# Kernel optimization log

Hardware: AMD Instinct MI355X
Metric: run time of the kernel (lower is better)

Reference implementation:

```python
import jax, jax.numpy as jnp
import numpy as np

N_ATOMS = 393216   # 4096 molecules * ~96 atoms
N_FEAT = 128
NB_FILTER = 128
NB_AFFINE = 11     # max_deg(10) + 1 - min_deg(0)
BATCH = 4096


def setup_inputs() -> dict:
    key = jax.random.key(0)
    k1, k2, k3, k4 = jax.random.split(key, 4)
    atoms = jax.random.normal(k1, (N_ATOMS, N_FEAT), jnp.float32)
    # stacked per-degree affine weights (glorot-ish scale)
    W = jax.random.normal(k2, (NB_AFFINE, N_FEAT, NB_FILTER), jnp.float32) / jnp.sqrt(jnp.float32(N_FEAT))
    b = jax.random.normal(k3, (NB_AFFINE, NB_FILTER), jnp.float32) * 0.01
    # contiguous degree layout: deg_slice[k] = (start, count), atoms sorted by degree
    counts = np.full(NB_AFFINE, N_ATOMS // NB_AFFINE, dtype=np.int32)
    counts[-1] += N_ATOMS - counts.sum()
    starts = np.concatenate([[0], np.cumsum(counts)[:-1]]).astype(np.int32)
    deg_slice = jnp.asarray(np.stack([starts, counts], axis=1))  # (11, 2) int32
    membership = jax.random.randint(k4, (N_ATOMS,), 0, BATCH, dtype=jnp.int32)
    return {"atoms": atoms, "W": W, "b": b, "deg_slice": deg_slice,
            "membership": membership, "batch_size": BATCH}


def reference(atoms, W, b, deg_slice, membership, batch_size):
    # atoms: (N, F); W: (K, F, O); b: (K, O); deg_slice: (K, 2)
    n = atoms.shape[0]
    nb_affine = W.shape[0]
    # Per-atom degree index from contiguous deg_slice layout:
    # deg_idx[i] = number of degree blocks that end at or before atom i.
    ends = jnp.cumsum(deg_slice[:, 1])                     # (K,)
    idx = jnp.arange(n, dtype=ends.dtype)
    deg_idx = jnp.sum(idx[:, None] >= ends[None, :], axis=1)  # (N,)
    # Per-degree affine: each atom uses the (W, b) of its degree block.
    out = jnp.zeros((n, W.shape[2]), dtype=atoms.dtype)
    for k in range(nb_affine):  # fixed small structural loop (11 distinct weight sets)
        yk = atoms @ W[k] + b[k]
        out = out + jnp.where((deg_idx == k)[:, None], yk, jnp.zeros((), atoms.dtype))
    # graph_gather: dynamic_partition + per-partition reduce_sum + concat == segment_sum
    pooled = jax.ops.segment_sum(out, membership, num_segments=batch_size)  # (B, O)
    # activation is 'linear' (identity); dropout is None
    return pooled
```

## Files before the change

### kernel.cpp

```cpp
#include <hip/hip_runtime.h>
#include <hip/hip_bf16.h>


#define CAP 64

typedef short bf16x8 __attribute__((ext_vector_type(8)));
typedef float f32x4  __attribute__((ext_vector_type(4)));

__device__ __forceinline__ unsigned short f2bf(float f) {
    unsigned int u = __builtin_bit_cast(unsigned int, f);
    u += 0x7fffu + ((u >> 16) & 1u);
    return (unsigned short)(u >> 16);
}

__device__ __forceinline__ int deg_of(int i, const int* __restrict__ ds, int K) {
    int k = 0, end = 0;
    for (int kk = 0; kk < K; ++kk) { end += ds[2 * kk + 1]; k += (i >= end) ? 1 : 0; }
    return k;
}

__global__ __launch_bounds__(256) void k_fill_wconv(
    const int* __restrict__ mem, const int* __restrict__ ds,
    const float* __restrict__ W,
    unsigned* __restrict__ cnt, unsigned* __restrict__ slots,
    unsigned short* __restrict__ Wb, int N, int K, int nb)
{
    int bx = blockIdx.x;
    if (bx >= nb) {
        __shared__ unsigned short t[128 * 130];
        int k = bx - nb;
        const float* Wk = W + (size_t)k * 16384;
        unsigned short* Wbk = Wb + (size_t)k * 16384;
        for (int e = threadIdx.x; e < 16384; e += 256) {
            int f = e >> 7, c = e & 127;
            t[f * 130 + c] = f2bf(Wk[e]);
        }
        __syncthreads();
        for (int e = threadIdx.x; e < 16384; e += 256) {
            int c = e >> 7, f = e & 127;
            Wbk[e] = t[f * 130 + c];
        }
        return;
    }
    int i = bx * 256 + threadIdx.x;
    if (i >= N) return;
    int key = mem[i] * K + deg_of(i, ds, K);
    unsigned p = atomicAdd(&cnt[key], 1u);
    if (p < CAP) slots[(size_t)key * CAP + p] = (unsigned)i;
}

__device__ __forceinline__ float4 f4add(float4 a, float4 b) {
    return make_float4(a.x + b.x, a.y + b.y, a.z + b.z, a.w + b.w);
}

__global__ __launch_bounds__(256) void k_phaseA(
    const float* __restrict__ atoms,
    const unsigned* __restrict__ cnt,
    const unsigned* __restrict__ slots,
    unsigned short* __restrict__ S, int KB)
{
    int bin = blockIdx.x * 4 + (threadIdx.x >> 6);
    if (bin >= KB) return;
    int lane = threadIdx.x & 63;
    int rpar = lane >> 5;
    int f4   = lane & 31;
    int n = (int)cnt[bin];
    if (n > CAP) n = CAP;
    const unsigned* sl = slots + (size_t)bin * CAP;

    float4 A0 = make_float4(0.f, 0.f, 0.f, 0.f);
    float4 A1 = A0, A2 = A0, A3 = A0;
    int j = rpar;
    for (; j + 6 < n; j += 8) {
        unsigned r0 = sl[j], r1 = sl[j + 2], r2 = sl[j + 4], r3 = sl[j + 6];
        float4 v0 = *reinterpret_cast<const float4*>(atoms + (size_t)r0 * 128 + f4 * 4);
        float4 v1 = *reinterpret_cast<const float4*>(atoms + (size_t)r1 * 128 + f4 * 4);
        float4 v2 = *reinterpret_cast<const float4*>(atoms + (size_t)r2 * 128 + f4 * 4);
        float4 v3 = *reinterpret_cast<const float4*>(atoms + (size_t)r3 * 128 + f4 * 4);
        A0 = f4add(A0, v0); A1 = f4add(A1, v1);
        A2 = f4add(A2, v2); A3 = f4add(A3, v3);
    }
    for (; j < n; j += 2) {
        float4 v = *reinterpret_cast<const float4*>(atoms + (size_t)sl[j] * 128 + f4 * 4);
        A0 = f4add(A0, v);
    }
    float4 Sm = f4add(f4add(A0, A1), f4add(A2, A3));
    Sm.x += __shfl_xor(Sm.x, 32, 64);
    Sm.y += __shfl_xor(Sm.y, 32, 64);
    Sm.z += __shfl_xor(Sm.z, 32, 64);
    Sm.w += __shfl_xor(Sm.w, 32, 64);
    if (rpar == 0) {
        unsigned lo = (unsigned)f2bf(Sm.x) | ((unsigned)f2bf(Sm.y) << 16);
        unsigned hi = (unsigned)f2bf(Sm.z) | ((unsigned)f2bf(Sm.w) << 16);
        *reinterpret_cast<uint2*>(S + (size_t)bin * 128 + f4 * 4) = make_uint2(lo, hi);
    }
}

__global__ __launch_bounds__(64) void k_phaseB(
    const unsigned short* __restrict__ S,
    const unsigned short* __restrict__ Wb,
    const unsigned* __restrict__ cnt,
    const float* __restrict__ bias,
    float* __restrict__ out,
    int K)
{
    int bx   = blockIdx.x;
    int s0   = (bx >> 2) * 16;
    int c0   = (bx & 3) * 32;
    int lane = threadIdx.x;
    int quad = lane >> 4, cb = lane & 15;

    const int KD = K * 128;
    f32x4 acc0 = (f32x4){0.f, 0.f, 0.f, 0.f};
    f32x4 acc1 = (f32x4){0.f, 0.f, 0.f, 0.f};

    const unsigned short* Arow = S  + (size_t)(s0 + cb) * KD + quad * 8;
    const unsigned short* B0   = Wb + (size_t)(c0 + cb)      * 128 + quad * 8;
    const unsigned short* B1   = Wb + (size_t)(c0 + 16 + cb) * 128 + quad * 8;

    #pragma unroll 1
    for (int kk = 0; kk < K; ++kk) {
        #pragma unroll
        for (int k0 = 0; k0 < 128; k0 += 32) {
            bf16x8 a  = *reinterpret_cast<const bf16x8*>(Arow + kk * 128 + k0);
            bf16x8 b0 = *reinterpret_cast<const bf16x8*>(B0 + (size_t)kk * 16384 + k0);
            bf16x8 b1 = *reinterpret_cast<const bf16x8*>(B1 + (size_t)kk * 16384 + k0);
            acc0 = __builtin_amdgcn_mfma_f32_16x16x32_bf16(a, b0, acc0, 0, 0, 0);
            acc1 = __builtin_amdgcn_mfma_f32_16x16x32_bf16(a, b1, acc1, 0, 0, 0);
        }
    }
    #pragma unroll
    for (int reg = 0; reg < 4; ++reg) {
        int s = s0 + quad * 4 + reg;
        float b0s = 0.f, b1s = 0.f;
        for (int k = 0; k < K; ++k) {
            float c = (float)cnt[(size_t)s * K + k];
            b0s += c * bias[k * 128 + c0 + cb];
            b1s += c * bias[k * 128 + c0 + 16 + cb];
        }
        out[(size_t)s * 128 + c0 + cb]      = acc0[reg] + b0s;
        out[(size_t)s * 128 + c0 + 16 + cb] = acc1[reg] + b1s;
    }
}

#define TM 64
#define LDA 136
#define LDW 136
__global__ __launch_bounds__(256, 2) void degree_affine_pool(
    const float* __restrict__ atoms, const float* __restrict__ W,
    const float* __restrict__ bias, const int* __restrict__ deg_slice,
    const int* __restrict__ membership, float* __restrict__ out, int K)
{
    __shared__ unsigned short Alds[TM * LDA];
    __shared__ unsigned short Wlds[128 * LDW];
    const int bid = blockIdx.x, tid = threadIdx.x;
    int k = -1, tile = 0, acc_t = 0;
    for (int kk = 0; kk < K; ++kk) {
        int c = deg_slice[2 * kk + 1];
        int nt = (c + TM - 1) >> 6;
        if (k < 0 && bid < acc_t + nt) { k = kk; tile = bid - acc_t; }
        acc_t += nt;
    }
    if (k < 0) return;
    const int start = deg_slice[2 * k], cnt = deg_slice[2 * k + 1];
    const int row0 = start + tile * TM;
    const int rows_valid = min(TM, cnt - tile * TM);
    for (int e = tid; e < TM * 32; e += 256) {
        int r = e >> 5, f4 = e & 31;
        float4 v = make_float4(0.f, 0.f, 0.f, 0.f);
        if (r < rows_valid)
            v = *reinterpret_cast<const float4*>(atoms + (size_t)(row0 + r) * 128 + f4 * 4);
        unsigned lo = (unsigned)f2bf(v.x) | ((unsigned)f2bf(v.y) << 16);
        unsigned hi = (unsigned)f2bf(v.z) | ((unsigned)f2bf(v.w) << 16);
        *reinterpret_cast<uint2*>(&Alds[r * LDA + f4 * 4]) = make_uint2(lo, hi);
    }
    const float* Wk = W + (size_t)k * 16384;
    for (int e = tid; e < 8192; e += 256) {
        int c = e & 127, f2 = e >> 7;
        unsigned p = (unsigned)f2bf(Wk[(2 * f2) * 128 + c]) |
                     ((unsigned)f2bf(Wk[(2 * f2 + 1) * 128 + c]) << 16);
        *reinterpret_cast<unsigned*>(&Wlds[c * LDW + 2 * f2]) = p;
    }
    __syncthreads();
    const int wave = tid >> 6, lane = tid & 63, quad = lane >> 4, cb = lane & 15;
    f32x4 acc[8];
    #pragma unroll
    for (int ct = 0; ct < 8; ++ct) acc[ct] = (f32x4){0.f, 0.f, 0.f, 0.f};
    #pragma unroll
    for (int k0 = 0; k0 < 128; k0 += 32) {
        bf16x8 af = *reinterpret_cast<const bf16x8*>(&Alds[(wave * 16 + cb) * LDA + k0 + quad * 8]);
        #pragma unroll
        for (int ct = 0; ct < 8; ++ct) {
            bf16x8 bf = *reinterpret_cast<const bf16x8*>(&Wlds[(ct * 16 + cb) * LDW + k0 + quad * 8]);
            acc[ct] = __builtin_amdgcn_mfma_f32_16x16x32_bf16(af, bf, acc[ct], 0, 0, 0);
        }
    }
    int segs[4]; bool valid[4];
    #pragma unroll
    for (int reg = 0; reg < 4; ++reg) {
        int rl = wave * 16 + quad * 4 + reg;
        valid[reg] = (rl < rows_valid);
        segs[reg] = valid[reg] ? membership[row0 + rl] : 0;
    }
    const float* bk = bias + k * 128;
    #pragma unroll
    for (int ct = 0; ct < 8; ++ct) {
        int col = ct * 16 + cb;
        float bv = bk[col];
        #pragma unroll
        for (int reg = 0; reg < 4; ++reg)
            if (valid[reg])
                __hip_atomic_fetch_add(out + (size_t)segs[reg] * 128 + col,
                                       acc[ct][reg] + bv, __ATOMIC_RELAXED,
                                       __HIP_MEMORY_SCOPE_AGENT);
    }
}

static inline size_t aln(size_t x) { return (x + 255) & ~(size_t)255; }

extern "C" void kernel_launch(void* const* d_in, const int* in_sizes, int n_in,
                              void* d_out, int out_size, void* d_ws, size_t ws_size,
                              hipStream_t stream) {
    const float* atoms = (const float*)d_in[0];
    const float* W     = (const float*)d_in[1];
    const float* bias  = (const float*)d_in[2];
    const int*   deg   = (const int*)d_in[3];
    const int*   mem   = (const int*)d_in[4];
    float*       out   = (float*)d_out;

    const int K  = in_sizes[3] / 2;
    const int N  = in_sizes[0] / 128;
    const int B  = out_size / 128;
    const int KB = B * K;

    size_t oWb   = 0;                       size_t sWb   = (size_t)K * 16384 * 2;
    size_t oCnt  = aln(oWb + sWb);          size_t sCnt  = (size_t)KB * 4;
    size_t oSlot = aln(oCnt + sCnt);        size_t sSlot = (size_t)KB * CAP * 4;
    size_t oS    = aln(oSlot + sSlot);      size_t sS    = (size_t)KB * 128 * 2;
    size_t total = oS + sS;

    if (ws_size < total || (B & 15) != 0) {
        (void)hipMemsetAsync(d_out, 0, (size_t)out_size * sizeof(float), stream);
        const int blocks = (N + TM - 1) / TM + K;
        degree_affine_pool<<<blocks, 256, 0, stream>>>(atoms, W, bias, deg, mem, out, K);
        return;
    }

    char* ws = (char*)d_ws;
    unsigned short* Wb    = (unsigned short*)(ws + oWb);
    unsigned*       cnt   = (unsigned*)(ws + oCnt);
    unsigned*       slots = (unsigned*)(ws + oSlot);
    unsigned short* S     = (unsigned short*)(ws + oS);

    (void)hipMemsetAsync(cnt, 0, sCnt, stream);

    const int nb = (N + 255) / 256;
    k_fill_wconv<<<nb + K, 256, 0, stream>>>(mem, deg, W, cnt, slots, Wb, N, K, nb);
    k_phaseA    <<<(KB + 3) / 4, 256, 0, stream>>>(atoms, cnt, slots, S, KB);
    k_phaseB    <<<(B / 16) * 4, 64, 0, stream>>>(S, Wb, cnt, bias, out, K);
}
```

Baseline: 347.7 us.

## Fuse bin-fill, gather-sum and MFMA phases into one persistent kernel with grid barriers

Replaces three launches (fill/weight-convert, per-bin gather sum, MFMA GEMM) with one persistent 512-block kernel that separates the phases with atomic global barriers. The barrier counter is zeroed by the same memset as the counts. Slot indices for each bin are staged in LDS before the gather loop. The aim is to remove launch gaps and tail effects between kernels. The cost is fewer waves per phase, barrier spin overhead, and reliance on all 512 blocks being co-resident, which could deadlock if they are not.

Result: slower. 654.1 us (+88.1%).

```diff
diff --git a/kernel.cpp b/kernel.cpp
--- a/kernel.cpp
+++ b/kernel.cpp
@@ -2,7 +2,9 @@
 #include <hip/hip_bf16.h>
 
 
-#define CAP 64
+#define CAP  64
+#define GRID 512
+#define TPB  256
 
 typedef short bf16x8 __attribute__((ext_vector_type(8)));
 typedef float f32x4  __attribute__((ext_vector_type(4)));
@@ -19,127 +21,138 @@
     return k;
 }
 
-__global__ __launch_bounds__(256) void k_fill_wconv(
-    const int* __restrict__ mem, const int* __restrict__ ds,
-    const float* __restrict__ W,
-    unsigned* __restrict__ cnt, unsigned* __restrict__ slots,
-    unsigned short* __restrict__ Wb, int N, int K, int nb)
-{
-    int bx = blockIdx.x;
-    if (bx >= nb) {
-        __shared__ unsigned short t[128 * 130];
-        int k = bx - nb;
-        const float* Wk = W + (size_t)k * 16384;
-        unsigned short* Wbk = Wb + (size_t)k * 16384;
-        for (int e = threadIdx.x; e < 16384; e += 256) {
-            int f = e >> 7, c = e & 127;
-            t[f * 130 + c] = f2bf(Wk[e]);
-        }
-        __syncthreads();
-        for (int e = threadIdx.x; e < 16384; e += 256) {
-            int c = e >> 7, f = e & 127;
-            Wbk[e] = t[f * 130 + c];
-        }
-        return;
-    }
-    int i = bx * 256 + threadIdx.x;
-    if (i >= N) return;
-    int key = mem[i] * K + deg_of(i, ds, K);
-    unsigned p = atomicAdd(&cnt[key], 1u);
-    if (p < CAP) slots[(size_t)key * CAP + p] = (unsigned)i;
-}
-
 __device__ __forceinline__ float4 f4add(float4 a, float4 b) {
     return make_float4(a.x + b.x, a.y + b.y, a.z + b.z, a.w + b.w);
 }
 
-__global__ __launch_bounds__(256) void k_phaseA(
+__device__ __forceinline__ void gbar(unsigned* bar, unsigned target) {
+    __threadfence();
+    __syncthreads();
+    if (threadIdx.x == 0) {
+        __hip_atomic_fetch_add(bar, 1u, __ATOMIC_ACQ_REL, __HIP_MEMORY_SCOPE_AGENT);
+        while (__hip_atomic_load(bar, __ATOMIC_ACQUIRE, __HIP_MEMORY_SCOPE_AGENT) < target)
+            __builtin_amdgcn_s_sleep(2);
+    }
+    __syncthreads();
+    __threadfence();
+}
+
+__global__ __launch_bounds__(TPB, 2) void k_mega(
     const float* __restrict__ atoms,
-    const unsigned* __restrict__ cnt,
-    const unsigned* __restrict__ slots,
-    unsigned short* __restrict__ S, int KB)
+    const float* __restrict__ W,
+    const float* __restrict__ bias,
+    const int*   __restrict__ ds,
+    const int*   __restrict__ mem,
+    float*       __restrict__ out,
+    unsigned*    __restrict__ cnt,
+    unsigned*    __restrict__ slots,
+    unsigned short* __restrict__ Wb,
+    unsigned short* __restrict__ S,
+    unsigned*    __restrict__ bar,
+    int N, int K, int B)
 {
-    int bin = blockIdx.x * 4 + (threadIdx.x >> 6);
-    if (bin >= KB) return;
-    int lane = threadIdx.x & 63;
-    int rpar = lane >> 5;
-    int f4   = lane & 31;
-    int n = (int)cnt[bin];
-    if (n > CAP) n = CAP;
-    const unsigned* sl = slots + (size_t)bin * CAP;
-
-    float4 A0 = make_float4(0.f, 0.f, 0.f, 0.f);
-    float4 A1 = A0, A2 = A0, A3 = A0;
-    int j = rpar;
-    for (; j + 6 < n; j += 8) {
-        unsigned r0 = sl[j], r1 = sl[j + 2], r2 = sl[j + 4], r3 = sl[j + 6];
-        float4 v0 = *reinterpret_cast<const float4*>(atoms + (size_t)r0 * 128 + f4 * 4);
-        float4 v1 = *reinterpret_cast<const float4*>(atoms + (size_t)r1 * 128 + f4 * 4);
-        float4 v2 = *reinterpret_cast<const float4*>(atoms + (size_t)r2 * 128 + f4 * 4);
-        float4 v3 = *reinterpret_cast<const float4*>(atoms + (size_t)r3 * 128 + f4 * 4);
-        A0 = f4add(A0, v0); A1 = f4add(A1, v1);
-        A2 = f4add(A2, v2); A3 = f4add(A3, v3);
-    }
-    for (; j < n; j += 2) {
-        float4 v = *reinterpret_cast<const float4*>(atoms + (size_t)sl[j] * 128 + f4 * 4);
-        A0 = f4add(A0, v);
-    }
-    float4 Sm = f4add(f4add(A0, A1), f4add(A2, A3));
-    Sm.x += __shfl_xor(Sm.x, 32, 64);
-    Sm.y += __shfl_xor(Sm.y, 32, 64);
-    Sm.z += __shfl_xor(Sm.z, 32, 64);
-    Sm.w += __shfl_xor(Sm.w, 32, 64);
-    if (rpar == 0) {
-        unsigned lo = (unsigned)f2bf(Sm.x) | ((unsigned)f2bf(Sm.y) << 16);
-        unsigned hi = (unsigned)f2bf(Sm.z) | ((unsigned)f2bf(Sm.w) << 16);
-        *reinterpret_cast<uint2*>(S + (size_t)bin * 128 + f4 * 4) = make_uint2(lo, hi);
-    }
-}
-
-__global__ __launch_bounds__(64) void k_phaseB(
-    const unsigned short* __restrict__ S,
-    const unsigned short* __restrict__ Wb,
-    const unsigned* __restrict__ cnt,
-    const float* __restrict__ bias,
-    float* __restrict__ out,
-    int K)
-{
-    int bx   = blockIdx.x;
-    int s0   = (bx >> 2) * 16;
-    int c0   = (bx & 3) * 32;
-    int lane = threadIdx.x;
-    int quad = lane >> 4, cb = lane & 15;
-
+    __shared__ unsigned short wt[128 * 130];
+    __shared__ unsigned slbuf[TPB / 64][64];
+    const int bid = blockIdx.x, tid = threadIdx.x;
+    const int KB = B * K;
+
+    for (int i = bid * TPB + tid; i < N; i += GRID * TPB) {
+        int key = mem[i] * K + deg_of(i, ds, K);
+        unsigned p = atomicAdd(&cnt[key], 1u);
+        if (p < CAP) slots[(size_t)key * CAP + p] = (unsigned)i;
+    }
+    gbar(bar, GRID);
+
+    if (bid < K) {
+        const float* Wk = W + (size_t)bid * 16384;
+        unsigned short* Wbk = Wb + (size_t)bid * 16384;
+        for (int e = tid; e < 16384; e += TPB) {
+            int f = e >> 7, c = e & 127;
+            wt[f * 130 + c] = f2bf(Wk[e]);
+        }
+        __syncthreads();
+        for (int e = tid; e < 16384; e += TPB) {
+            int c = e >> 7, f = e & 127;
+            Wbk[e] = wt[f * 130 + c];
+        }
+    }
+
+    const int wv   = tid >> 6;
+    const int wid  = bid * (TPB / 64) + wv;
+    const int nw   = GRID * (TPB / 64);
+    const int lane = tid & 63;
+    const int rpar = lane >> 5;
+    const int f4   = lane & 31;
+    unsigned* sw = slbuf[wv];
+
+    for (int bin = wid; bin < KB; bin += nw) {
+        int n = (int)cnt[bin];
+        if (n > CAP) n = CAP;
+        sw[lane] = slots[(size_t)bin * CAP + lane];
+        float4 A0 = make_float4(0.f, 0.f, 0.f, 0.f);
+        float4 A1 = A0, A2 = A0, A3 = A0;
+        int j = rpar;
+        for (; j + 6 < n; j += 8) {
+            unsigned r0 = sw[j], r1 = sw[j + 2], r2 = sw[j + 4], r3 = sw[j + 6];
+            float4 v0 = *reinterpret_cast<const float4*>(atoms + (size_t)r0 * 128 + f4 * 4);
+            float4 v1 = *reinterpret_cast<const float4*>(atoms + (size_t)r1 * 128 + f4 * 4);
+            float4 v2 = *reinterpret_cast<const float4*>(atoms + (size_t)r2 * 128 + f4 * 4);
+            float4 v3 = *reinterpret_cast<const float4*>(atoms + (size_t)r3 * 128 + f4 * 4);
+            A0 = f4add(A0, v0); A1 = f4add(A1, v1);
+            A2 = f4add(A2, v2); A3 = f4add(A3, v3);
+        }
+        for (; j < n; j += 2) {
+            unsigned r = sw[j];
+            float4 v = *reinterpret_cast<const float4*>(atoms + (size_t)r * 128 + f4 * 4);
+            A0 = f4add(A0, v);
+        }
+        float4 Sm = f4add(f4add(A0, A1), f4add(A2, A3));
+        Sm.x += __shfl_xor(Sm.x, 32, 64);
+        Sm.y += __shfl_xor(Sm.y, 32, 64);
+        Sm.z += __shfl_xor(Sm.z, 32, 64);
+        Sm.w += __shfl_xor(Sm.w, 32, 64);
+        if (rpar == 0) {
+            unsigned lo = (unsigned)f2bf(Sm.x) | ((unsigned)f2bf(Sm.y) << 16);
+            unsigned hi = (unsigned)f2bf(Sm.z) | ((unsigned)f2bf(Sm.w) << 16);
+            *reinterpret_cast<uint2*>(S + (size_t)bin * 128 + f4 * 4) = make_uint2(lo, hi);
+        }
+    }
+    gbar(bar, 2u * GRID);
+
+    const int ntiles = (B / 16) * 4;
+    const int quad = lane >> 4, cb = lane & 15;
     const int KD = K * 128;
-    f32x4 acc0 = (f32x4){0.f, 0.f, 0.f, 0.f};
-    f32x4 acc1 = (f32x4){0.f, 0.f, 0.f, 0.f};
-
-    const unsigned short* Arow = S  + (size_t)(s0 + cb) * KD + quad * 8;
-    const unsigned short* B0   = Wb + (size_t)(c0 + cb)      * 128 + quad * 8;
-    const unsigned short* B1   = Wb + (size_t)(c0 + 16 + cb) * 128 + quad * 8;
-
-    #pragma unroll 1
-    for (int kk = 0; kk < K; ++kk) {
+    for (int t = wid; t < ntiles; t += nw) {
+        int s0 = (t >> 2) * 16;
+        int c0 = (t & 3) * 32;
+        f32x4 acc0 = (f32x4){0.f, 0.f, 0.f, 0.f};
+        f32x4 acc1 = (f32x4){0.f, 0.f, 0.f, 0.f};
+        const unsigned short* Arow = S  + (size_t)(s0 + cb) * KD + quad * 8;
+        const unsigned short* B0   = Wb + (size_t)(c0 + cb)      * 128 + quad * 8;
+        const unsigned short* B1   = Wb + (size_t)(c0 + 16 + cb) * 128 + quad * 8;
+        #pragma unroll 1
+        for (int kk = 0; kk < K; ++kk) {
+            #pragma unroll
+            for (int k0 = 0; k0 < 128; k0 += 32) {
+                bf16x8 a  = *reinterpret_cast<const bf16x8*>(Arow + kk * 128 + k0);
+                bf16x8 b0 = *reinterpret_cast<const bf16x8*>(B0 + (size_t)kk * 16384 + k0);
+                bf16x8 b1 = *reinterpret_cast<const bf16x8*>(B1 + (size_t)kk * 16384 + k0);
+                acc0 = __builtin_amdgcn_mfma_f32_16x16x32_bf16(a, b0, acc0, 0, 0, 0);
+                acc1 = __builtin_amdgcn_mfma_f32_16x16x32_bf16(a, b1, acc1, 0, 0, 0);
+            }
+        }
         #pragma unroll
-        for (int k0 = 0; k0 < 128; k0 += 32) {
-            bf16x8 a  = *reinterpret_cast<const bf16x8*>(Arow + kk * 128 + k0);
-            bf16x8 b0 = *reinterpret_cast<const bf16x8*>(B0 + (size_t)kk * 16384 + k0);
-            bf16x8 b1 = *reinterpret_cast<const bf16x8*>(B1 + (size_t)kk * 16384 + k0);
-            acc0 = __builtin_amdgcn_mfma_f32_16x16x32_bf16(a, b0, acc0, 0, 0, 0);
-            acc1 = __builtin_amdgcn_mfma_f32_16x16x32_bf16(a, b1, acc1, 0, 0, 0);
-        }
-    }
-    #pragma unroll
-    for (int reg = 0; reg < 4; ++reg) {
-        int s = s0 + quad * 4 + reg;
-        float b0s = 0.f, b1s = 0.f;
-        for (int k = 0; k < K; ++k) {
-            float c = (float)cnt[(size_t)s * K + k];
-            b0s += c * bias[k * 128 + c0 + cb];
-            b1s += c * bias[k * 128 + c0 + 16 + cb];
-        }
-        out[(size_t)s * 128 + c0 + cb]      = acc0[reg] + b0s;
-        out[(size_t)s * 128 + c0 + 16 + cb] = acc1[reg] + b1s;
+        for (int reg = 0; reg < 4; ++reg) {
+            int s = s0 + quad * 4 + reg;
+            float b0s = 0.f, b1s = 0.f;
+            for (int k = 0; k < K; ++k) {
+                float c = (float)cnt[(size_t)s * K + k];
+                b0s += c * bias[k * 128 + c0 + cb];
+                b1s += c * bias[k * 128 + c0 + 16 + cb];
+            }
+            out[(size_t)s * 128 + c0 + cb]      = acc0[reg] + b0s;
+            out[(size_t)s * 128 + c0 + 16 + cb] = acc1[reg] + b1s;
+        }
     }
 }
 
@@ -235,11 +248,12 @@
 
     size_t oWb   = 0;                       size_t sWb   = (size_t)K * 16384 * 2;
     size_t oCnt  = aln(oWb + sWb);          size_t sCnt  = (size_t)KB * 4;
-    size_t oSlot = aln(oCnt + sCnt);        size_t sSlot = (size_t)KB * CAP * 4;
+    size_t oBar  = aln(oCnt + sCnt);        size_t sBar  = 256;
+    size_t oSlot = aln(oBar + sBar);        size_t sSlot = (size_t)KB * CAP * 4;
     size_t oS    = aln(oSlot + sSlot);      size_t sS    = (size_t)KB * 128 * 2;
     size_t total = oS + sS;
 
-    if (ws_size < total || (B & 15) != 0) {
+    if (ws_size < total || (B & 15) != 0 || K > GRID) {
         (void)hipMemsetAsync(d_out, 0, (size_t)out_size * sizeof(float), stream);
         const int blocks = (N + TM - 1) / TM + K;
         degree_affine_pool<<<blocks, 256, 0, stream>>>(atoms, W, bias, deg, mem, out, K);
@@ -249,13 +263,12 @@
     char* ws = (char*)d_ws;
     unsigned short* Wb    = (unsigned short*)(ws + oWb);
     unsigned*       cnt   = (unsigned*)(ws + oCnt);
+    unsigned*       bar   = (unsigned*)(ws + oBar);
     unsigned*       slots = (unsigned*)(ws + oSlot);
     unsigned short* S     = (unsigned short*)(ws + oS);
 
-    (void)hipMemsetAsync(cnt, 0, sCnt, stream);
-
-    const int nb = (N + 255) / 256;
-    k_fill_wconv<<<nb + K, 256, 0, stream>>>(mem, deg, W, cnt, slots, Wb, N, K, nb);
-    k_phaseA    <<<(KB + 3) / 4, 256, 0, stream>>>(atoms, cnt, slots, S, KB);
-    k_phaseB    <<<(B / 16) * 4, 64, 0, stream>>>(S, Wb, cnt, bias, out, K);
-}
+    (void)hipMemsetAsync(cnt, 0, (oBar + sBar) - oCnt, stream);
+
+    k_mega<<<GRID, TPB, 0, stream>>>(atoms, W, bias, deg, mem, out,
+                                     cnt, slots, Wb, S, bar, N, K, B);
+}
```
